# Kernel optimization log

Measured on AMD Instinct MI355X. Metric: run time of the kernel, lower is better.

Reference implementation:

```python
import jax, jax.numpy as jnp
import numpy as np


def setup_inputs() -> dict:
    key = jax.random.key(0)
    ks = jax.random.split(key, 4)
    B, T, Z, FV = 128, 16, 33, 28 * 28
    return {
        "img": jax.random.uniform(ks[0], (B, 28, 28), dtype=jnp.float32),
        "whz": 0.05 * jax.random.normal(ks[1], (T, Z, FV), dtype=jnp.float32),
        "bias": 0.05 * jax.random.normal(ks[2], (1,), dtype=jnp.float32),
        "b_scale_out": jnp.zeros((), dtype=jnp.float32),
        "prior_tzz": 0.5 * jax.random.normal(ks[3], (T, Z, Z), dtype=jnp.float32),
        "M": 8,
        "nstep": 4,
    }


def reference(img, whz, bias, b_scale_out, prior_tzz, M, nstep):
    B = img.shape[0]
    T, Z, FV = whz.shape
    K = Z - 1
    x = img.reshape(B, FV)  # node_bx, treated as constant (detached in original)
    # disjoint pixel segments per latent slot t (partition [0, FV))
    sep = FV // T + 1
    vv = jnp.arange(FV)
    tt = jnp.arange(T)
    mask_tl = (vv[None, :] >= tt[:, None] * sep) & (vv[None, :] < (tt[:, None] + 1) * sep)  # (T, FV)
    scale = jnp.exp(b_scale_out)
    loc = whz + bias[0]  # (T, Z, FV)
    # Gaussian log-likelihood of each pixel under each (slot t, state z): (T, Z, B, FV)
    diff = (x[None, None, :, :] - loc[:, :, None, :]) / scale
    logn = -0.5 * diff * diff - jnp.log(scale) - 0.5 * jnp.log(2.0 * jnp.pi)
    # per-slot segment likelihood table lp_seg[t, z, b] = sum over pixels owned by slot t
    lp_seg = jnp.einsum('tzbv,tv->tzb', logn, mask_tl.astype(logn.dtype))  # (T, Z, B)
    lp_prior_log = jax.nn.log_softmax(prior_tzz, axis=-1)  # (T, Z, Z)

    t_idx = tt
    b_idx = jnp.arange(B)
    kk = jnp.arange(K)
    base_key = jax.random.key(42)

    def step(carry, i):
        xmz, lp_m = carry  # xmz: (B, M, T) int, lp_m: (B, M)
        t = i % T
        # K candidate assignments: copy of xmz with slot t replaced by k
        xkz = jnp.broadcast_to(xmz[:, :, None, :], (B, M, K, T))
        xkz = xkz.at[:, :, :, t].set(kk[None, None, :])
        # external (pixel) log-likelihood: sum_t lp_seg[t, z_t, b]
        lp_ext = lp_seg[t_idx[None, None, None, :], xkz, b_idx[:, None, None, None]].sum(-1)  # (B, M, K)
        # internal (Markov-chain prior), parent of slot 0 is state 0
        parents = jnp.concatenate([jnp.zeros((B, M, K, 1), xkz.dtype), xkz[..., :-1]], axis=-1)
        lp_int = lp_prior_log[t_idx[None, None, None, :], parents, xkz].sum(-1)  # (B, M, K)
        lp_total = lp_ext + lp_int
        idx_k = jax.random.categorical(jax.random.fold_in(base_key, i), lp_total, axis=-1)  # (B, M)
        lp_m = jnp.take_along_axis(lp_total, idx_k[..., None], axis=-1)[..., 0]
        xmz = xmz.at[:, :, t].set(idx_k)
        return (xmz, lp_m), None

    xmz0 = jnp.zeros((B, M, T), dtype=jnp.int32)
    lp_m0 = jnp.zeros((B, M), dtype=x.dtype)
    (xmz, lp_m), _ = jax.lax.scan(step, (xmz0, lp_m0), jnp.arange(nstep * T))
    lse = jax.nn.logsumexp(lp_m, axis=-1)  # (B,)
    return -lse.mean()
```

## Files before the change

### kernel.cpp

```cpp
#include <hip/hip_runtime.h>
#include <cstdint>

#define T_ 16
#define Z_ 33
#define K_ 32
#define FV_ 784
#define B_ 128
#define M_ 8
#define NSTEP_ 4
#define SEP_ 50
#define NOISE_N (64u * 32768u)

#define GN_OFF    0u
#define LPSEG_OFF 2097152u
#define PLW_OFF   (LPSEG_OFF + 67584u)
#define LPM_OFF   (PLW_OFF + 17424u)
#define WS_NEED_BYTES ((size_t)(LPM_OFF + 1024u + 16u) * 4)

__device__ __forceinline__ uint32_t rotl32(uint32_t v, int r) {
  return (v << r) | (v >> (32 - r));
}

__device__ __forceinline__ void tf2x32(uint32_t k0, uint32_t k1,
                                       uint32_t& x0, uint32_t& x1) {
  uint32_t k2 = k0 ^ k1 ^ 0x1BD11BDAu;
  x0 += k0; x1 += k1;
#define RND_(r) { x0 += x1; x1 = rotl32(x1, r); x1 ^= x0; }
  RND_(13) RND_(15) RND_(26) RND_(6)
  x0 += k1; x1 += k2 + 1u;
  RND_(17) RND_(29) RND_(16) RND_(24)
  x0 += k2; x1 += k0 + 2u;
  RND_(13) RND_(15) RND_(26) RND_(6)
  x0 += k0; x1 += k1 + 3u;
  RND_(17) RND_(29) RND_(16) RND_(24)
  x0 += k1; x1 += k2 + 4u;
  RND_(13) RND_(15) RND_(26) RND_(6)
  x0 += k2; x1 += k0 + 5u;
#undef RND_
}

__device__ __forceinline__ float gumbel_fast(uint32_t bits) {
  const float TINY = 1.17549435e-38f;
  float u = __uint_as_float((bits >> 9) | 0x3F800000u) - 1.0f;
  u = fmaxf(TINY, u * (1.0f - TINY) + TINY);
  return -__logf(-__logf(u));
}

__device__ __forceinline__ float gumbel_bits(uint32_t bits) {
  const float TINY = 1.17549435e-38f;
  float u = __uint_as_float((bits >> 9) | 0x3F800000u) - 1.0f;
  u = fmaxf(TINY, u * (1.0f - TINY) + TINY);
  return -logf(-logf(u));
}

template <int CTRL>
__device__ __forceinline__ float dpp_f(float x) {
  int xi = __float_as_int(x);
  int r = __builtin_amdgcn_update_dpp(xi, xi, CTRL, 0xF, 0xF, false);
  return __int_as_float(r);
}


__global__ __launch_bounds__(256) void ZBML3_prep2lean(
    const float* __restrict__ img, const float* __restrict__ whz,
    const float* __restrict__ bias_p, const float* __restrict__ bso_p,
    const float* __restrict__ prior, float* __restrict__ ws,
    float* __restrict__ out) {
  const int bid = blockIdx.x, tid = threadIdx.x;
  float* gn = ws + GN_OFF;
  float* lpseg = ws + LPSEG_OFF;
  float* plw = ws + PLW_OFF;
  if (bid < 1024) {
    const uint32_t g = (uint32_t)(bid * 256 + tid);
    const uint32_t i = g >> 12;
    const uint32_t jb = g & 4095u;
    uint32_t k0 = 0u, k1 = i;
    tf2x32(0u, 42u, k0, k1);
    float* out_g = gn + (size_t)i * 32768u;
#pragma unroll
    for (uint32_t jj = 0; jj < 4; ++jj) {
      uint32_t j = jb + jj * 4096u;
      uint32_t x0 = j, x1 = j + 16384u;
      tf2x32(k0, k1, x0, x1);
      out_g[j] = gumbel_fast(x0);
      out_g[j + 16384u] = gumbel_fast(x1);
    }
  } else if (bid < 1024 + 528) {
    const int e = bid - 1024;
    if (tid < B_) {
      const int b = tid;
      const float bias0 = bias_p[0];
      const float scale = __expf(bso_p[0]);
      const float con = -__logf(scale) - 0.9189385332046727f;
      const int t = e / 33;
      const int v0 = t * SEP_;
      const int v1 = (v0 + SEP_ < FV_) ? v0 + SEP_ : FV_;
      const int nv2 = (v1 - v0) >> 1;
      const float2* wp2 = (const float2*)(whz + (size_t)e * FV_ + v0);
      const float2* xp2 = (const float2*)(img + (size_t)b * FV_ + v0);
      float acc = 0.0f;
      for (int j = 0; j < nv2; ++j) {
        float2 xv = xp2[j], wv = wp2[j];
        float d0 = (xv.x - (wv.x + bias0)) / scale;
        acc += -0.5f * d0 * d0;
        float d1 = (xv.y - (wv.y + bias0)) / scale;
        acc += -0.5f * d1 * d1;
      }
      lpseg[b * 528 + e] = acc + (float)(v1 - v0) * con;
    }
  } else if (bid < 1555) {
    const int r = (bid - 1552) * 256 + tid;
    if (r < 528) {
      const float* pr = prior + r * 33;
      float mx = pr[0];
      for (int z = 1; z < 33; ++z) mx = fmaxf(mx, pr[z]);
      float sse = 0.0f;
      for (int z = 0; z < 33; ++z) sse += __expf(pr[z] - mx);
      float lg = __logf(sse);
      for (int z = 0; z < 33; ++z) plw[r * 33 + z] = pr[z] - mx - lg;
    }
  } else {
    if (tid == 0) out[0] = 0.0f;
  }
}

__global__ __launch_bounds__(256) void ZBML3_gibbs7(
    const float* __restrict__ gn, const float* __restrict__ lpseg,
    const float* __restrict__ plw_g, float* __restrict__ out) {
  __shared__ float pl[T_ * 1089];
  __shared__ float sseg[528];

  const int b = blockIdx.x;
  const int tid = threadIdx.x;
  const int k = tid & 31;
  const int m = tid >> 5;
  const int half = m & 1;
  const uint32_t idx = (uint32_t)(b * 256 + tid);

  {
    const float4* src = (const float4*)plw_g;
    float4* dst = (float4*)pl;
#pragma unroll
    for (int it = 0; it < 17; ++it) {
      int j = it * 256 + tid;
      if (j < 4356) dst[j] = src[j];
    }
    const float4* ss = (const float4*)(lpseg + b * 528);
    float4* dd = (float4*)sseg;
    if (tid < 132) dd[tid] = ss[tid];
  }

  float g0[T_];
#pragma unroll
  for (int t = 0; t < T_; ++t) g0[t] = gn[(size_t)t * 32768u + idx];

  __syncthreads();

  float sl[T_];
#pragma unroll
  for (int t = 0; t < T_; ++t) sl[t] = sseg[t * 33 + k];

  int s[T_];
#pragma unroll
  for (int t = 0; t < T_; ++t) s[t] = 0;

  float c[T_];
#pragma unroll
  for (int t = 0; t < T_; ++t) {
    float pn = (t < T_ - 1) ? pl[(t + 1) * 1089 + k * 33] : 0.0f;
    c[t] = g0[t] + sl[t] + pn;
  }

#pragma unroll
  for (int w = 0; w < NSTEP_; ++w) {
    if (w < NSTEP_ - 1) {
#pragma unroll
      for (int t = 0; t < T_; ++t)
        g0[t] = gn[(size_t)((w + 1) * 16 + t) * 32768u + idx];
    }
#pragma unroll
    for (int t = 0; t < T_; ++t) {
      const int p = (t == 0) ? 0 : s[t - 1];
      float v = c[t] + pl[t * 1089 + p * 33 + k];
      float rm = v;
      rm = fmaxf(rm, dpp_f<0x121>(rm));
      rm = fmaxf(rm, dpp_f<0x122>(rm));
      rm = fmaxf(rm, dpp_f<0x124>(rm));
      rm = fmaxf(rm, dpp_f<0x128>(rm));
      float bc = dpp_f<0x142>(rm);
      float m2 = fmaxf(rm, bc);
      int mAi = __builtin_amdgcn_readlane(__float_as_int(m2), 31);
      int mBi = __builtin_amdgcn_readlane(__float_as_int(m2), 63);
      float vmax = __int_as_float(half == 0 ? mAi : mBi);
      unsigned long long ball = __ballot(v == vmax);
      int kA = __ffs((unsigned int)ball) - 1;
      int kB = __ffs((unsigned int)(ball >> 32)) - 1;
      s[t] = (half == 0) ? kA : kB;
    }
    if (w < NSTEP_ - 1) {
#pragma unroll
      for (int t = 0; t < T_; ++t) {
        float pn = (t < T_ - 1) ? pl[(t + 1) * 1089 + k * 33 + s[t + 1]] : 0.0f;
        c[t] = g0[t] + sl[t] + pn;
      }
    }
  }

  float lpf = 0.0f;
  int prev = 0;
#pragma unroll
  for (int t = 0; t < T_; ++t) {
    lpf += sseg[t * 33 + s[t]] + pl[t * 1089 + prev * 33 + s[t]];
    prev = s[t];
  }

  __syncthreads();
  if (k == 0) sseg[m] = lpf;
  __syncthreads();
  if (tid == 0) {
    float mx = sseg[0];
#pragma unroll
    for (int mm = 1; mm < M_; ++mm) mx = fmaxf(mx, sseg[mm]);
    float sse = 0.0f;
#pragma unroll
    for (int mm = 0; mm < M_; ++mm) sse += __expf(sseg[mm] - mx);
    float lse = mx + __logf(sse);
    atomicAdd(out, -lse * (1.0f / 128.0f));
  }
}


__global__ __launch_bounds__(256) void ZBML3_gibbs_kernel(
    const float* __restrict__ img, const float* __restrict__ whz,
    const float* __restrict__ bias_p, const float* __restrict__ bso_p,
    const float* __restrict__ prior, float* __restrict__ lse_out) {
  __shared__ float pl[T_ * Z_ * Z_];
  __shared__ float slseg[T_ * Z_];
  __shared__ float xrow[FV_];
  __shared__ uint32_t key0s[NSTEP_ * T_], key1s[NSTEP_ * T_];
  __shared__ float lpm[M_];

  const int b = blockIdx.x;
  const int tid = threadIdx.x;
  const float bias0 = bias_p[0];
  const float scale = expf(bso_p[0]);
  const float con = -logf(scale) - 0.9189385332046727f;

  for (int v = tid; v < FV_; v += 256) xrow[v] = img[b * FV_ + v];
  __syncthreads();

  for (int e = tid; e < T_ * Z_; e += 256) {
    int t = e / Z_;
    int v0 = t * SEP_;
    int v1 = v0 + SEP_ < FV_ ? v0 + SEP_ : FV_;
    float acc = 0.0f;
    const float* wp = whz + (size_t)e * FV_;
    for (int v = v0; v < v1; ++v) {
      float d = (xrow[v] - (wp[v] + bias0)) / scale;
      acc += -0.5f * d * d;
    }
    slseg[e] = acc + (float)(v1 - v0) * con;
  }
  for (int r = tid; r < T_ * Z_; r += 256) {
    const float* pr = prior + r * Z_;
    float mx = pr[0];
    for (int z = 1; z < Z_; ++z) mx = fmaxf(mx, pr[z]);
    float sse = 0.0f;
    for (int z = 0; z < Z_; ++z) sse += expf(pr[z] - mx);
    float lg = logf(sse);
    for (int z = 0; z < Z_; ++z) pl[r * Z_ + z] = pr[z] - mx - lg;
  }
  if (tid < NSTEP_ * T_) {
    uint32_t x0 = 0u, x1 = (uint32_t)tid;
    tf2x32(0u, 42u, x0, x1);
    key0s[tid] = x0; key1s[tid] = x1;
  }
  __syncthreads();

  const int m = tid >> 5;
  const int k = tid & 31;
  const uint32_t idx = (uint32_t)(b * 256 + tid);
  const uint32_t jctr = idx & 16383u;
  const bool sel0 = idx < 16384u;

  int s[T_];
#pragma unroll
  for (int t = 0; t < T_; ++t) s[t] = 0;

  for (int sweep = 0; sweep < NSTEP_; ++sweep) {
#pragma unroll
    for (int t = 0; t < T_; ++t) {
      const int i = sweep * T_ + t;
      const uint32_t kk0 = key0s[i], kk1 = key1s[i];
      const int p = (t == 0) ? 0 : s[t - 1];
      float lp = slseg[t * Z_ + k] + pl[t * Z_ * Z_ + p * Z_ + k];
      if (t < T_ - 1) lp += pl[(t + 1) * Z_ * Z_ + k * Z_ + s[t + 1]];
      uint32_t x0 = jctr, x1 = jctr + 16384u;
      tf2x32(kk0, kk1, x0, x1);
      float g = gumbel_bits(sel0 ? x0 : x1);
      float val = lp + g;
      int ki = k;
      for (int d = 16; d > 0; d >>= 1) {
        float ov = __shfl_xor(val, d);
        int oi = __shfl_xor(ki, d);
        if (ov > val || (ov == val && oi < ki)) { val = ov; ki = oi; }
      }
      s[t] = ki;
    }
  }

  float lpf = 0.0f;
  int prev = 0;
#pragma unroll
  for (int t = 0; t < T_; ++t) {
    lpf += slseg[t * Z_ + s[t]] + pl[t * Z_ * Z_ + prev * Z_ + s[t]];
    prev = s[t];
  }
  if (k == 0) lpm[m] = lpf;
  __syncthreads();
  if (tid == 0) {
    float mx = lpm[0];
    for (int mm = 1; mm < M_; ++mm) mx = fmaxf(mx, lpm[mm]);
    float sse = 0.0f;
    for (int mm = 0; mm < M_; ++mm) sse += expf(lpm[mm] - mx);
    lse_out[b] = mx + logf(sse);
  }
}

__global__ __launch_bounds__(128) void ZBML3_reduce_kernel(
    const float* __restrict__ lse, float* __restrict__ out) {
  __shared__ float sm[B_];
  const int tid = threadIdx.x;
  sm[tid] = lse[tid];
  __syncthreads();
  if (tid == 0) {
    float s = 0.0f;
    for (int i = 0; i < B_; ++i) s += sm[i];
    out[0] = -(s / (float)B_);
  }
}

extern "C" void kernel_launch(void* const* d_in, const int* in_sizes, int n_in,
                              void* d_out, int out_size, void* d_ws, size_t ws_size,
                              hipStream_t stream) {
  const float* img   = (const float*)d_in[0];
  const float* whz   = (const float*)d_in[1];
  const float* bias  = (const float*)d_in[2];
  const float* bso   = (const float*)d_in[3];
  const float* prior = (const float*)d_in[4];

  if (ws_size >= WS_NEED_BYTES) {
    float* ws = (float*)d_ws;
    ZBML3_prep2lean<<<1556, 256, 0, stream>>>(img, whz, bias, bso, prior, ws,
                                              (float*)d_out);
    ZBML3_gibbs7<<<B_, 256, 0, stream>>>(ws + GN_OFF, ws + LPSEG_OFF,
                                         ws + PLW_OFF, (float*)d_out);
  } else {
    float* lse = (float*)d_ws;
    ZBML3_gibbs_kernel<<<B_, 256, 0, stream>>>(img, whz, bias, bso, prior, lse);
    ZBML3_reduce_kernel<<<1, B_, 0, stream>>>(lse, (float*)d_out);
  }
}
```

Before: 32.36 us.

## Generate Gumbel noise inline in Gibbs kernel instead of precomputing to workspace

Removes the 2M-element Gumbel noise buffer that the prep kernel wrote to global memory and the Gibbs kernel read back. Per-step Threefry keys are now computed once per block into shared memory, and each thread generates only the one noise value it needs, right when it is used. This cuts about 1000 blocks from the prep launch and removes the noise traffic in both directions. In exchange, Threefry arithmetic now sits on the serial Gibbs kernel's path, which runs on only 128 blocks.

```diff
diff --git a/kernel.cpp b/kernel.cpp
--- a/kernel.cpp
+++ b/kernel.cpp
@@ -9,13 +9,10 @@
 #define M_ 8
 #define NSTEP_ 4
 #define SEP_ 50
-#define NOISE_N (64u * 32768u)
-
-#define GN_OFF    0u
-#define LPSEG_OFF 2097152u
-#define PLW_OFF   (LPSEG_OFF + 67584u)
-#define LPM_OFF   (PLW_OFF + 17424u)
-#define WS_NEED_BYTES ((size_t)(LPM_OFF + 1024u + 16u) * 4)
+
+#define LPSEG_OFF 0u
+#define PLW_OFF   67584u
+#define WS_NEED_BYTES ((size_t)(PLW_OFF + 17424u + 1040u) * 4)
 
 __device__ __forceinline__ uint32_t rotl32(uint32_t v, int r) {
   return (v << r) | (v >> (32 - r));
@@ -61,32 +58,16 @@
 }
 
 
-__global__ __launch_bounds__(256) void ZBML3_prep2lean(
+__global__ __launch_bounds__(256) void ZBML3_prep3(
     const float* __restrict__ img, const float* __restrict__ whz,
     const float* __restrict__ bias_p, const float* __restrict__ bso_p,
     const float* __restrict__ prior, float* __restrict__ ws,
     float* __restrict__ out) {
   const int bid = blockIdx.x, tid = threadIdx.x;
-  float* gn = ws + GN_OFF;
   float* lpseg = ws + LPSEG_OFF;
   float* plw = ws + PLW_OFF;
-  if (bid < 1024) {
-    const uint32_t g = (uint32_t)(bid * 256 + tid);
-    const uint32_t i = g >> 12;
-    const uint32_t jb = g & 4095u;
-    uint32_t k0 = 0u, k1 = i;
-    tf2x32(0u, 42u, k0, k1);
-    float* out_g = gn + (size_t)i * 32768u;
-#pragma unroll
-    for (uint32_t jj = 0; jj < 4; ++jj) {
-      uint32_t j = jb + jj * 4096u;
-      uint32_t x0 = j, x1 = j + 16384u;
-      tf2x32(k0, k1, x0, x1);
-      out_g[j] = gumbel_fast(x0);
-      out_g[j + 16384u] = gumbel_fast(x1);
-    }
-  } else if (bid < 1024 + 528) {
-    const int e = bid - 1024;
+  if (bid < 528) {
+    const int e = bid;
     if (tid < B_) {
       const int b = tid;
       const float bias0 = bias_p[0];
@@ -108,8 +89,8 @@
       }
       lpseg[b * 528 + e] = acc + (float)(v1 - v0) * con;
     }
-  } else if (bid < 1555) {
-    const int r = (bid - 1552) * 256 + tid;
+  } else if (bid < 531) {
+    const int r = (bid - 528) * 256 + tid;
     if (r < 528) {
       const float* pr = prior + r * 33;
       float mx = pr[0];
@@ -124,11 +105,12 @@
   }
 }
 
-__global__ __launch_bounds__(256) void ZBML3_gibbs7(
-    const float* __restrict__ gn, const float* __restrict__ lpseg,
-    const float* __restrict__ plw_g, float* __restrict__ out) {
+__global__ __launch_bounds__(256) void ZBML3_gibbs8(
+    const float* __restrict__ lpseg, const float* __restrict__ plw_g,
+    float* __restrict__ out) {
   __shared__ float pl[T_ * 1089];
   __shared__ float sseg[528];
+  __shared__ uint32_t key0s[64], key1s[64];
 
   const int b = blockIdx.x;
   const int tid = threadIdx.x;
@@ -136,6 +118,14 @@
   const int m = tid >> 5;
   const int half = m & 1;
   const uint32_t idx = (uint32_t)(b * 256 + tid);
+  const uint32_t j0 = idx & 16383u;
+  const bool sel0 = idx < 16384u;
+
+  if (tid < 64) {
+    uint32_t x0 = 0u, x1 = (uint32_t)tid;
+    tf2x32(0u, 42u, x0, x1);
+    key0s[tid] = x0; key1s[tid] = x1;
+  }
 
   {
     const float4* src = (const float4*)plw_g;
@@ -150,15 +140,19 @@
     if (tid < 132) dd[tid] = ss[tid];
   }
 
+  __syncthreads();
+
+  float sl[T_];
+#pragma unroll
+  for (int t = 0; t < T_; ++t) sl[t] = sseg[t * 33 + k];
+
   float g0[T_];
 #pragma unroll
-  for (int t = 0; t < T_; ++t) g0[t] = gn[(size_t)t * 32768u + idx];
-
-  __syncthreads();
-
-  float sl[T_];
-#pragma unroll
-  for (int t = 0; t < T_; ++t) sl[t] = sseg[t * 33 + k];
+  for (int t = 0; t < T_; ++t) {
+    uint32_t x0 = j0, x1 = j0 + 16384u;
+    tf2x32(key0s[t], key1s[t], x0, x1);
+    g0[t] = gumbel_fast(sel0 ? x0 : x1);
+  }
 
   int s[T_];
 #pragma unroll
@@ -175,8 +169,12 @@
   for (int w = 0; w < NSTEP_; ++w) {
     if (w < NSTEP_ - 1) {
 #pragma unroll
-      for (int t = 0; t < T_; ++t)
-        g0[t] = gn[(size_t)((w + 1) * 16 + t) * 32768u + idx];
+      for (int t = 0; t < T_; ++t) {
+        const int i = (w + 1) * 16 + t;
+        uint32_t x0 = j0, x1 = j0 + 16384u;
+        tf2x32(key0s[i], key1s[i], x0, x1);
+        g0[t] = gumbel_fast(sel0 ? x0 : x1);
+      }
     }
 #pragma unroll
     for (int t = 0; t < T_; ++t) {
@@ -351,10 +349,10 @@
 
   if (ws_size >= WS_NEED_BYTES) {
     float* ws = (float*)d_ws;
-    ZBML3_prep2lean<<<1556, 256, 0, stream>>>(img, whz, bias, bso, prior, ws,
-                                              (float*)d_out);
-    ZBML3_gibbs7<<<B_, 256, 0, stream>>>(ws + GN_OFF, ws + LPSEG_OFF,
-                                         ws + PLW_OFF, (float*)d_out);
+    ZBML3_prep3<<<532, 256, 0, stream>>>(img, whz, bias, bso, prior, ws,
+                                         (float*)d_out);
+    ZBML3_gibbs8<<<B_, 256, 0, stream>>>(ws + LPSEG_OFF, ws + PLW_OFF,
+                                         (float*)d_out);
   } else {
     float* lse = (float*)d_ws;
     ZBML3_gibbs_kernel<<<B_, 256, 0, stream>>>(img, whz, bias, bso, prior, lse);
```

New measurement: 39.99 us. 23.6% more time.
